# Kernel tuning notes

Hardware: AMD Instinct MI355X
Metric: run time of the kernel (lower is better)

## Reference

```python
import jax, jax.numpy as jnp
import numpy as np

D_MODEL = 1024
NUM_HEADS = 16
HEAD_DIM = D_MODEL // NUM_HEADS
SEQ_LEN = 2048
THETA = 10000.0


def setup_inputs() -> dict:
    key = jax.random.key(0)
    ks = jax.random.split(key, 9)
    s = 1.0 / np.sqrt(D_MODEL)
    inp = {
        "x": jax.random.normal(ks[0], (2, SEQ_LEN, D_MODEL), dtype=jnp.float32),
        "Wq": jax.random.uniform(ks[1], (D_MODEL, D_MODEL), jnp.float32, -s, s),
        "bq": jax.random.uniform(ks[2], (D_MODEL,), jnp.float32, -s, s),
        "Wk": jax.random.uniform(ks[3], (D_MODEL, D_MODEL), jnp.float32, -s, s),
        "bk": jax.random.uniform(ks[4], (D_MODEL,), jnp.float32, -s, s),
        "Wv": jax.random.uniform(ks[5], (D_MODEL, D_MODEL), jnp.float32, -s, s),
        "bv": jax.random.uniform(ks[6], (D_MODEL,), jnp.float32, -s, s),
        "Wo": jax.random.uniform(ks[7], (D_MODEL, D_MODEL), jnp.float32, -s, s),
        "bo": jax.random.uniform(ks[8], (D_MODEL,), jnp.float32, -s, s),
    }
    return inp


def _rope_cos_sin(seq_len, dim, theta):
    inv_freq = 1.0 / theta ** (jnp.arange(0, dim, 2, dtype=jnp.float32) / dim)  # [dim/2]
    t = jnp.arange(seq_len, dtype=jnp.float32)
    freqs = jnp.outer(t, inv_freq)  # [S, dim/2]
    return jnp.cos(freqs), jnp.sin(freqs)


def _apply_rope(x, cos, sin):
    # x: [B, H, S, head_dim]; interleaved complex pairs (even, odd)
    x2 = x.reshape(*x.shape[:-1], -1, 2)  # [B,H,S,hd/2,2]
    xe, xo = x2[..., 0], x2[..., 1]
    c = cos[None, None, :, :]
    s = sin[None, None, :, :]
    oe = xe * c - xo * s
    oo = xe * s + xo * c
    return jnp.stack([oe, oo], axis=-1).reshape(x.shape)


def reference(x, Wq, bq, Wk, bk, Wv, bv, Wo, bo):
    B, S, D = x.shape
    H, hd = NUM_HEADS, HEAD_DIM
    q = x @ Wq.T + bq
    k = x @ Wk.T + bk
    v = x @ Wv.T + bv
    # [B, H, S, hd]
    q = q.reshape(B, S, H, hd).transpose(0, 2, 1, 3)
    k = k.reshape(B, S, H, hd).transpose(0, 2, 1, 3)
    v = v.reshape(B, S, H, hd).transpose(0, 2, 1, 3)
    cos, sin = _rope_cos_sin(S, hd, THETA)
    q = _apply_rope(q, cos, sin)
    k = _apply_rope(k, cos, sin)
    scores = jnp.einsum("bhqd,bhkd->bhqk", q, k) / jnp.sqrt(jnp.float32(hd))
    causal = jnp.triu(jnp.ones((S, S), dtype=bool), k=1)
    scores = jnp.where(causal[None, None, :, :], -jnp.inf, scores)
    attn = jax.nn.softmax(scores, axis=-1)
    out = jnp.einsum("bhqk,bhkd->bhqd", attn, v)
    out = out.transpose(0, 2, 1, 3).reshape(B, S, D)
    return out @ Wo.T + bo
```

## Files before the change

### kernel.cpp

```cpp
#include <hip/hip_runtime.h>
#include <hip/hip_bf16.h>

#define S_LEN 2048
#define DM 1024
#define NH 16
#define HD 64
#define M_ROWS 4096
#define LOG2E 1.4426950408889634f
#define MASKVAL -1.0e4f
#define QSCALE 0.18033688011112042f

typedef __attribute__((ext_vector_type(8))) short short8;
typedef __attribute__((ext_vector_type(4))) float f32x4;
typedef __attribute__((ext_vector_type(16))) float f32x16;

__device__ inline ushort f2b(float f) {
  union { float f; unsigned u; } v; v.f = f;
  unsigned r = v.u + 0x7fffu + ((v.u >> 16) & 1u);
  return (ushort)(r >> 16);
}

__device__ inline float b2f(ushort u) {
  union { unsigned u; float f; } v; v.u = ((unsigned)u) << 16; return v.f;
}

__device__ inline unsigned pk_bf16(float a, float b) {
  __hip_bfloat162 h = __float22bfloat162_rn(make_float2(a, b));
  union { __hip_bfloat162 h; unsigned u; } v; v.h = h;
  return v.u;
}

__device__ inline float fexp2(float x) { return __builtin_amdgcn_exp2f(x); }

__device__ inline void gl_lds16(const void* g, void* l) {
  __builtin_amdgcn_global_load_lds(
      (const __attribute__((address_space(1))) void*)g,
      (__attribute__((address_space(3))) void*)l, 16, 0, 0);
}

__global__ __launch_bounds__(256) void cast_rope_kernel(
    const float* __restrict__ x, const float* __restrict__ Wq, const float* __restrict__ Wk,
    const float* __restrict__ Wv, const float* __restrict__ Wo,
    ushort* __restrict__ xb, ushort* __restrict__ Wqb, ushort* __restrict__ Wkb,
    ushort* __restrict__ Wvb, ushort* __restrict__ Wob,
    float* __restrict__ ropeC, float* __restrict__ ropeS) {
  const int bid = blockIdx.x;
  if (bid >= 8192) {
    int idx = (bid - 8192) * 256 + threadIdx.x;
    int s = idx >> 5, i = idx & 31;
    float inv = exp2f(-(float)i * (13.287712379549449f / 32.0f));
    float a = (float)s * inv;
    ropeC[idx] = cosf(a);
    ropeS[idx] = sinf(a);
    return;
  }
  int i = bid * 256 + threadIdx.x;
  int r = i >> 18, off = i & 0x3FFFF;
  const float4* s;
  uint2* d;
  switch (r) {
    case 0: case 1: case 2: case 3: s = (const float4*)x + i;  d = (uint2*)xb + i;  break;
    case 4: s = (const float4*)Wq + off; d = (uint2*)Wqb + off; break;
    case 5: s = (const float4*)Wk + off; d = (uint2*)Wkb + off; break;
    case 6: s = (const float4*)Wv + off; d = (uint2*)Wvb + off; break;
    default: s = (const float4*)Wo + off; d = (uint2*)Wob + off; break;
  }
  float4 v = *s;
  uint2 o;
  o.x = pk_bf16(v.x, v.y);
  o.y = pk_bf16(v.z, v.w);
  *d = o;
}

__global__ __launch_bounds__(256) void gemm_qkv_kernel(const ushort* __restrict__ xb,
    const ushort* __restrict__ Wqb, const ushort* __restrict__ Wkb, const ushort* __restrict__ Wvb,
    const float* __restrict__ bq, const float* __restrict__ bk, const float* __restrict__ bv,
    const float* __restrict__ ropeC, const float* __restrict__ ropeS,
    ushort* __restrict__ qb, ushort* __restrict__ kb, ushort* __restrict__ vT) {
  __shared__ ushort lds[17408];
  ushort* As = lds;
  ushort* Bs = lds + 8192;
  const int z = blockIdx.z;
  const ushort* W = (z == 0) ? Wqb : ((z == 1) ? Wkb : Wvb);
  const float* bias = (z == 0) ? bq : ((z == 1) ? bk : bv);
  const int m0 = blockIdx.x * 128, n0 = blockIdx.y * 128;
  const int t = threadIdx.x, lane = t & 63, wave = t >> 6;
  const int wr = (wave >> 1) * 64, wc = (wave & 1) * 64;
  const int lr = lane & 15, lg = lane >> 4;

  const int slot0 = wave * 128 + lane, slot1 = slot0 + 64;
  const int row0 = slot0 >> 2, g0 = (slot0 & 3) ^ (row0 & 3);
  const int row1 = slot1 >> 2, g1 = (slot1 & 3) ^ (row1 & 3);
  const ushort* Ap0 = &xb[(size_t)(m0 + row0) * DM + g0 * 8];
  const ushort* Ap1 = &xb[(size_t)(m0 + row1) * DM + g1 * 8];
  const ushort* Wp0 = &W[(size_t)(n0 + row0) * DM + g0 * 8];
  const ushort* Wp1 = &W[(size_t)(n0 + row1) * DM + g1 * 8];

  f32x4 acc[4][4];
#pragma unroll
  for (int a = 0; a < 4; a++)
#pragma unroll
    for (int b = 0; b < 4; b++) acc[a][b] = (f32x4){0.f, 0.f, 0.f, 0.f};

  gl_lds16(Ap0, &As[slot0 * 8]);
  gl_lds16(Ap1, &As[slot1 * 8]);
  gl_lds16(Wp0, &Bs[slot0 * 8]);
  gl_lds16(Wp1, &Bs[slot1 * 8]);
  __syncthreads();

  int buf = 0;
  for (int i = 0; i < 32; i++) {
    if (i + 1 < 32) {
      const int k0 = (i + 1) * 32;
      const int bo = (buf ^ 1) * 4096;
      gl_lds16(Ap0 + k0, &As[bo + slot0 * 8]);
      gl_lds16(Ap1 + k0, &As[bo + slot1 * 8]);
      gl_lds16(Wp0 + k0, &Bs[bo + slot0 * 8]);
      gl_lds16(Wp1 + k0, &Bs[bo + slot1 * 8]);
    }
    const int fb = buf * 4096;
    short8 af[4], bf[4];
#pragma unroll
    for (int mt = 0; mt < 4; mt++) {
      const int row = wr + mt * 16 + lr;
      af[mt] = *(const short8*)&As[fb + (row * 4 + (lg ^ (row & 3))) * 8];
    }
#pragma unroll
    for (int nt = 0; nt < 4; nt++) {
      const int row = wc + nt * 16 + lr;
      bf[nt] = *(const short8*)&Bs[fb + (row * 4 + (lg ^ (row & 3))) * 8];
    }
#pragma unroll
    for (int mt = 0; mt < 4; mt++)
#pragma unroll
      for (int nt = 0; nt < 4; nt++)
        acc[mt][nt] = __builtin_amdgcn_mfma_f32_16x16x32_bf16(af[mt], bf[nt], acc[mt][nt], 0, 0, 0);
    __syncthreads();
    buf ^= 1;
  }

#pragma unroll
  for (int mt = 0; mt < 4; mt++) {
#pragma unroll
    for (int nt = 0; nt < 4; nt++) {
      const int nloc = wc + nt * 16 + lr;
      const float bn = bias[n0 + nloc];
#pragma unroll
      for (int r = 0; r < 4; r++) {
        const int mloc = wr + mt * 16 + lg * 4 + r;
        const ushort v = f2b(acc[mt][nt][r] + bn);
        if (z < 2) lds[mloc * 136 + nloc] = v;
        else       lds[nloc * 136 + mloc] = v;
      }
    }
  }
  __syncthreads();

  const int b = m0 >> 11;
  if (z < 2) {
    ushort* dst = (z == 0) ? qb : kb;
    const float qscale = (z == 0) ? QSCALE : 1.0f;
#pragma unroll
    for (int c = 0; c < 8; c++) {
      const int sloc = c * 16 + (t >> 4);
      const int nloc = (t & 15) * 8;
      short8 val = *(const short8*)&lds[sloc * 136 + nloc];
      const int s = (m0 + sloc) & (S_LEN - 1);
      const int h = (n0 + nloc) >> 6;
      const int d0 = nloc & 63;
      const float4 cv = *(const float4*)&ropeC[s * 32 + d0 / 2];
      const float4 sv = *(const float4*)&ropeS[s * 32 + d0 / 2];
      uint4 o;
      {
        float e = b2f((ushort)val[0]), od = b2f((ushort)val[1]);
        o.x = pk_bf16((e * cv.x - od * sv.x) * qscale, (e * sv.x + od * cv.x) * qscale);
      }
      {
        float e = b2f((ushort)val[2]), od = b2f((ushort)val[3]);
        o.y = pk_bf16((e * cv.y - od * sv.y) * qscale, (e * sv.y + od * cv.y) * qscale);
      }
      {
        float e = b2f((ushort)val[4]), od = b2f((ushort)val[5]);
        o.z = pk_bf16((e * cv.z - od * sv.z) * qscale, (e * sv.z + od * cv.z) * qscale);
      }
      {
        float e = b2f((ushort)val[6]), od = b2f((ushort)val[7]);
        o.w = pk_bf16((e * cv.w - od * sv.w) * qscale, (e * sv.w + od * cv.w) * qscale);
      }
      *(uint4*)&dst[(((size_t)b * NH + h) * S_LEN + s) * HD + d0] = o;
    }
  } else {
    const int sbase = m0 & (S_LEN - 1);
#pragma unroll
    for (int c = 0; c < 8; c++) {
      const int nloc = c * 16 + (t >> 4);
      const int s0 = (t & 15) * 8;
      short8 val = *(const short8*)&lds[nloc * 136 + s0];
      const int h = (n0 + nloc) >> 6;
      const int d = nloc & 63;
      *(short8*)&vT[(((size_t)b * NH + h) * HD + d) * S_LEN + sbase + s0] = val;
    }
  }
}

__global__ __launch_bounds__(256) void flash_kernel(const ushort* __restrict__ qb,
                                                    const ushort* __restrict__ kb,
                                                    const ushort* __restrict__ vT,
                                                    ushort* __restrict__ Oh,
                                                    float* __restrict__ lsum) {
  __shared__ ushort Ks[2][4096];
  __shared__ ushort VTs[2][4096];
  const int t = threadIdx.x, lane = t & 63, wave = t >> 6;
  const int q31 = lane & 31, h = lane >> 5;
  const int bh = blockIdx.y;
  const int cid = blockIdx.x;
  const int g = (cid >= 24) ? 3 : (cid >= 12) ? 2 : (cid >= 4) ? 1 : 0;
  const int nc = g + 1;
  const int o = cid - 4 * ((g * (g + 1)) >> 1);
  const int qi = o / nc;
  const int c = o - qi * nc;
  const int qt = g * 4 + qi;
  const int q0 = qt * 128;
  const int ntiles = 2 * qt + 2;
  const int kstart = c * 8;
  const int kend = min(kstart + 8, ntiles);
  const int pidx = bh * 40 + cid;

  const ushort* kbh = kb + (size_t)bh * S_LEN * HD;
  const ushort* vbh = vT + (size_t)bh * HD * S_LEN;

  const int qrow = q0 + wave * 32 + q31;
  const ushort* qptr = qb + ((size_t)bh * S_LEN + qrow) * HD + h * 8;
  short8 qf[4];
#pragma unroll
  for (int s = 0; s < 4; s++) qf[s] = *(const short8*)(qptr + s * 16);

  const int slot0 = wave * 128 + lane, slot1 = slot0 + 64;
  const int row0 = slot0 >> 3, g0 = (slot0 & 7) ^ (row0 & 7);
  const int row1 = slot1 >> 3, g1 = (slot1 & 7) ^ (row1 & 7);
  const int lo0 = wave * 128 * 8, lo1 = lo0 + 64 * 8;

  int foff[4][2];
#pragma unroll
  for (int s = 0; s < 4; s++)
#pragma unroll
    for (int st = 0; st < 2; st++) {
      const int row = st * 32 + q31;
      foff[s][st] = (row * 8 + ((2 * s + h) ^ (row & 7))) * 8;
    }

  {
    const int k00 = kstart * 64;
    gl_lds16(kbh + (size_t)(k00 + row0) * HD + g0 * 8, &Ks[0][lo0]);
    gl_lds16(kbh + (size_t)(k00 + row1) * HD + g1 * 8, &Ks[0][lo1]);
    gl_lds16(vbh + (size_t)row0 * S_LEN + k00 + g0 * 8, &VTs[0][lo0]);
    gl_lds16(vbh + (size_t)row1 * S_LEN + k00 + g1 * 8, &VTs[0][lo1]);
  }
  __syncthreads();

  f32x16 O[2];
#pragma unroll
  for (int st = 0; st < 2; st++)
#pragma unroll
    for (int r = 0; r < 16; r++) O[st][r] = 0.f;
  float lacc = 0.f;
  int cur = 0;

  for (int kt = kstart; kt < kend; kt++) {
    if (kt + 1 < kend) {
      const int k0n = (kt + 1) * 64;
      gl_lds16(kbh + (size_t)(k0n + row0) * HD + g0 * 8, &Ks[cur ^ 1][lo0]);
      gl_lds16(kbh + (size_t)(k0n + row1) * HD + g1 * 8, &Ks[cur ^ 1][lo1]);
      gl_lds16(vbh + (size_t)row0 * S_LEN + k0n + g0 * 8, &VTs[cur ^ 1][lo0]);
      gl_lds16(vbh + (size_t)row1 * S_LEN + k0n + g1 * 8, &VTs[cur ^ 1][lo1]);
    }
    const ushort* Kb = Ks[cur];
    const ushort* Vb = VTs[cur];

    f32x16 sc[2];
#pragma unroll
    for (int st = 0; st < 2; st++)
#pragma unroll
      for (int r = 0; r < 16; r++) sc[st][r] = 0.f;
#pragma unroll
    for (int s = 0; s < 4; s++) {
#pragma unroll
      for (int st = 0; st < 2; st++) {
        const short8 kf = *(const short8*)&Kb[foff[s][st]];
        sc[st] = __builtin_amdgcn_mfma_f32_32x32x16_bf16(kf, qf[s], sc[st], 0, 0, 0);
      }
    }
    if (kt * 64 + 63 > q0 + wave * 32) {
#pragma unroll
      for (int st = 0; st < 2; st++)
#pragma unroll
        for (int r = 0; r < 16; r++) {
          const int kcol = kt * 64 + st * 32 + (r & 3) + 8 * (r >> 2) + 4 * h;
          if (kcol > qrow) sc[st][r] = MASKVAL;
        }
    }
#pragma unroll
    for (int st = 0; st < 2; st++)
#pragma unroll
      for (int r = 0; r < 16; r++) {
        const float p = fexp2(sc[st][r]);
        sc[st][r] = p;
        lacc += p;
      }

    unsigned pp[8][2];
#pragma unroll
    for (int st = 0; st < 2; st++)
#pragma unroll
      for (int rg = 0; rg < 4; rg++) {
        pp[st * 4 + rg][0] = pk_bf16(sc[st][4 * rg + 0], sc[st][4 * rg + 1]);
        pp[st * 4 + rg][1] = pk_bf16(sc[st][4 * rg + 2], sc[st][4 * rg + 3]);
      }
#pragma unroll
    for (int s = 0; s < 4; s++) {
      const unsigned sA0 = pp[2 * s][0], sA1 = pp[2 * s][1];
      const unsigned sB0 = pp[2 * s + 1][0], sB1 = pp[2 * s + 1][1];
      const unsigned send0 = h ? sA0 : sB0;
      const unsigned send1 = h ? sA1 : sB1;
      const unsigned recv0 = (unsigned)__shfl_xor((int)send0, 32);
      const unsigned recv1 = (unsigned)__shfl_xor((int)send1, 32);
      union { unsigned u[4]; short8 v; } pf;
      pf.u[0] = h ? recv0 : sA0;
      pf.u[1] = h ? recv1 : sA1;
      pf.u[2] = h ? sB0 : recv0;
      pf.u[3] = h ? sB1 : recv1;
#pragma unroll
      for (int st = 0; st < 2; st++) {
        const short8 vf = *(const short8*)&Vb[foff[s][st]];
        O[st] = __builtin_amdgcn_mfma_f32_32x32x16_bf16(vf, pf.v, O[st], 0, 0, 0);
      }
    }
    __syncthreads();
    cur ^= 1;
  }

  lacc += __shfl_xor(lacc, 32);

  ushort* obase = Oh + ((size_t)pidx * 128 + wave * 32 + q31) * HD;
#pragma unroll
  for (int st = 0; st < 2; st++)
#pragma unroll
    for (int rg = 0; rg < 4; rg++) {
      const int d0 = st * 32 + 8 * rg + 4 * h;
      uint2 w;
      w.x = pk_bf16(O[st][4 * rg + 0], O[st][4 * rg + 1]);
      w.y = pk_bf16(O[st][4 * rg + 2], O[st][4 * rg + 3]);
      *(uint2*)&obase[d0] = w;
    }
  if (h == 0) lsum[(size_t)pidx * 128 + wave * 32 + q31] = lacc;
}

__global__ __launch_bounds__(256) void combine_kernel(const ushort* __restrict__ Oh,
                                                      const float* __restrict__ lsum,
                                                      ushort* __restrict__ attn) {
  const int tid = blockIdx.x * 256 + threadIdx.x;
  const int d8 = tid & 7;
  const int q = (tid >> 3) & (S_LEN - 1);
  const int bh = tid >> 14;
  const int qt = q >> 7, row = q & 127;
  const int g = qt >> 2, nc = g + 1;
  const int base = 4 * ((g * (g + 1)) >> 1) + (qt & 3) * nc;
  const int p0 = bh * 40 + base;

  float l = 0.f;
  float acc[8];
#pragma unroll
  for (int j = 0; j < 8; j++) acc[j] = 0.f;
  for (int c = 0; c < nc; c++) {
    const size_t rowidx = (size_t)(p0 + c) * 128 + row;
    l += lsum[rowidx];
    const uint4 a = *(const uint4*)&Oh[rowidx * HD + d8 * 8];
    const unsigned au[4] = {a.x, a.y, a.z, a.w};
#pragma unroll
    for (int j = 0; j < 4; j++) {
      acc[2 * j] += b2f((ushort)(au[j] & 0xffff));
      acc[2 * j + 1] += b2f((ushort)(au[j] >> 16));
    }
  }
  const float inv = 1.f / l;
  uint4 o;
  unsigned* op = (unsigned*)&o;
#pragma unroll
  for (int j = 0; j < 4; j++) op[j] = pk_bf16(acc[2 * j] * inv, acc[2 * j + 1] * inv);
  const int b = bh >> 4, hh = bh & 15;
  *(uint4*)&attn[((size_t)b * S_LEN + q) * DM + hh * HD + d8 * 8] = o;
}

__global__ __launch_bounds__(256) void gemm_out_kernel(const ushort* __restrict__ attn,
                                                       const ushort* __restrict__ Wob,
                                                       const float* __restrict__ bo,
                                                       float* __restrict__ out) {
  __shared__ ushort As[2][4096];
  __shared__ ushort Bs[2][2048];
  const int m0 = blockIdx.x * 128, n0 = blockIdx.y * 64;
  const int t = threadIdx.x, lane = t & 63, wave = t >> 6;
  const int wm = (wave >> 1) * 64, wn = (wave & 1) * 32;
  const int lr = lane & 15, lg = lane >> 4;
  const int slotA0 = wave * 128 + lane, slotA1 = slotA0 + 64;
  const int rowA0 = slotA0 >> 2, gA0 = (slotA0 & 3) ^ (rowA0 & 3);
  const int rowA1 = slotA1 >> 2, gA1 = (slotA1 & 3) ^ (rowA1 & 3);
  const int slotB = wave * 64 + lane;
  const int rowB = slotB >> 2, gB = (slotB & 3) ^ (rowB & 3);
  const ushort* Ap0 = &attn[(size_t)(m0 + rowA0) * DM + gA0 * 8];
  const ushort* Ap1 = &attn[(size_t)(m0 + rowA1) * DM + gA1 * 8];
  const ushort* Wp  = &Wob[(size_t)(n0 + rowB) * DM + gB * 8];

  f32x4 acc[4][2];
#pragma unroll
  for (int a = 0; a < 4; a++)
#pragma unroll
    for (int b = 0; b < 2; b++) acc[a][b] = (f32x4){0.f, 0.f, 0.f, 0.f};

  gl_lds16(Ap0, &As[0][slotA0 * 8]);
  gl_lds16(Ap1, &As[0][slotA1 * 8]);
  gl_lds16(Wp, &Bs[0][slotB * 8]);
  __syncthreads();

  int buf = 0;
  for (int i = 0; i < 32; i++) {
    if (i + 1 < 32) {
      const int k0 = (i + 1) * 32;
      gl_lds16(Ap0 + k0, &As[buf ^ 1][slotA0 * 8]);
      gl_lds16(Ap1 + k0, &As[buf ^ 1][slotA1 * 8]);
      gl_lds16(Wp + k0, &Bs[buf ^ 1][slotB * 8]);
    }
    short8 af[4], bf[2];
#pragma unroll
    for (int mt = 0; mt < 4; mt++) {
      const int row = wm + mt * 16 + lr;
      af[mt] = *(const short8*)&As[buf][(row * 4 + (lg ^ (row & 3))) * 8];
    }
#pragma unroll
    for (int nt = 0; nt < 2; nt++) {
      const int row = wn + nt * 16 + lr;
      bf[nt] = *(const short8*)&Bs[buf][(row * 4 + (lg ^ (row & 3))) * 8];
    }
#pragma unroll
    for (int mt = 0; mt < 4; mt++)
#pragma unroll
      for (int nt = 0; nt < 2; nt++)
        acc[mt][nt] = __builtin_amdgcn_mfma_f32_16x16x32_bf16(af[mt], bf[nt], acc[mt][nt], 0, 0, 0);
    __syncthreads();
    buf ^= 1;
  }

#pragma unroll
  for (int mt = 0; mt < 4; mt++) {
#pragma unroll
    for (int nt = 0; nt < 2; nt++) {
      const int n = n0 + wn + nt * 16 + lr;
      const float bn = bo[n];
#pragma unroll
      for (int r = 0; r < 4; r++) {
        const int m = m0 + wm + mt * 16 + lg * 4 + r;
        out[(size_t)m * DM + n] = acc[mt][nt][r] + bn;
      }
    }
  }
}

extern "C" void kernel_launch(void* const* d_in, const int* in_sizes, int n_in,
                              void* d_out, int out_size, void* d_ws, size_t ws_size,
                              hipStream_t stream) {
  const float* x  = (const float*)d_in[0];
  const float* Wq = (const float*)d_in[1];
  const float* bq = (const float*)d_in[2];
  const float* Wk = (const float*)d_in[3];
  const float* bk = (const float*)d_in[4];
  const float* Wv = (const float*)d_in[5];
  const float* bv = (const float*)d_in[6];
  const float* Wo = (const float*)d_in[7];
  const float* bo = (const float*)d_in[8];
  float* out = (float*)d_out;

  char* ws = (char*)d_ws;
  size_t off = 0;
  auto alloc = [&](size_t bytes) { char* p = ws + off; off += (bytes + 255) & ~255ull; return p; };
  ushort* xb   = (ushort*)alloc((size_t)M_ROWS * DM * 2);
  ushort* Wqb  = (ushort*)alloc((size_t)DM * DM * 2);
  ushort* Wkb  = (ushort*)alloc((size_t)DM * DM * 2);
  ushort* Wvb  = (ushort*)alloc((size_t)DM * DM * 2);
  ushort* Wob  = (ushort*)alloc((size_t)DM * DM * 2);
  ushort* qb   = (ushort*)alloc((size_t)M_ROWS * DM * 2);
  ushort* kb   = (ushort*)alloc((size_t)M_ROWS * DM * 2);
  ushort* vTb  = (ushort*)alloc((size_t)M_ROWS * DM * 2);
  ushort* attn = (ushort*)alloc((size_t)M_ROWS * DM * 2);
  ushort* Ohb  = (ushort*)alloc((size_t)1280 * 128 * HD * 2);
  float* lsb   = (float*)alloc((size_t)1280 * 128 * 4);
  float* ropeC = (float*)alloc((size_t)S_LEN * 32 * 4);
  float* ropeS = (float*)alloc((size_t)S_LEN * 32 * 4);
  (void)ws_size; (void)in_sizes; (void)n_in; (void)out_size;

  cast_rope_kernel<<<8448, 256, 0, stream>>>(x, Wq, Wk, Wv, Wo, xb, Wqb, Wkb, Wvb, Wob,
                                             ropeC, ropeS);
  gemm_qkv_kernel<<<dim3(M_ROWS / 128, DM / 128, 3), 256, 0, stream>>>(
      xb, Wqb, Wkb, Wvb, bq, bk, bv, ropeC, ropeS, qb, kb, vTb);
  flash_kernel<<<dim3(40, 32), 256, 0, stream>>>(qb, kb, vTb, Ohb, lsb);
  combine_kernel<<<2048, 256, 0, stream>>>(Ohb, lsb, attn);
  gemm_out_kernel<<<dim3(M_ROWS / 128, DM / 64), 256, 0, stream>>>(attn, Wob, bo, out);
}
```

Before: 192.4 us.

## Unroll flash loop by two with static LDS offsets, permlane swap, and setprio

Rewrites the flash attention inner loop as a macro unrolled twice, so the double-buffer offsets into one flat LDS array become compile-time constants. Global pointers now advance by increment instead of being recomputed each tile. The cross-half exchange of P values uses v_permlane32_swap instead of two shuffles plus selects. s_setprio is raised around the MFMA blocks and the row sums are accumulated in packed two-wide vectors. The aim is lower address and exchange overhead and better MFMA issue. The risks are higher register pressure, and the tile count per block must be even because the second body in each pair runs without a bounds check.

Result: no change. 190.7 us (-0.9%).

```diff
diff --git a/kernel.cpp b/kernel.cpp
--- a/kernel.cpp
+++ b/kernel.cpp
@@ -11,6 +11,7 @@
 #define QSCALE 0.18033688011112042f
 
 typedef __attribute__((ext_vector_type(8))) short short8;
+typedef __attribute__((ext_vector_type(2))) float f32x2;
 typedef __attribute__((ext_vector_type(4))) float f32x4;
 typedef __attribute__((ext_vector_type(16))) float f32x16;
 
@@ -208,8 +209,7 @@
                                                     const ushort* __restrict__ vT,
                                                     ushort* __restrict__ Oh,
                                                     float* __restrict__ lsum) {
-  __shared__ ushort Ks[2][4096];
-  __shared__ ushort VTs[2][4096];
+  __shared__ ushort lds[16384];
   const int t = threadIdx.x, lane = t & 63, wave = t >> 6;
   const int q31 = lane & 31, h = lane >> 5;
   const int bh = blockIdx.y;
@@ -251,11 +251,15 @@
 
   {
     const int k00 = kstart * 64;
-    gl_lds16(kbh + (size_t)(k00 + row0) * HD + g0 * 8, &Ks[0][lo0]);
-    gl_lds16(kbh + (size_t)(k00 + row1) * HD + g1 * 8, &Ks[0][lo1]);
-    gl_lds16(vbh + (size_t)row0 * S_LEN + k00 + g0 * 8, &VTs[0][lo0]);
-    gl_lds16(vbh + (size_t)row1 * S_LEN + k00 + g1 * 8, &VTs[0][lo1]);
-  }
+    gl_lds16(kbh + (size_t)(k00 + row0) * HD + g0 * 8, &lds[0 + lo0]);
+    gl_lds16(kbh + (size_t)(k00 + row1) * HD + g1 * 8, &lds[0 + lo1]);
+    gl_lds16(vbh + (size_t)row0 * S_LEN + k00 + g0 * 8, &lds[8192 + lo0]);
+    gl_lds16(vbh + (size_t)row1 * S_LEN + k00 + g1 * 8, &lds[8192 + lo1]);
+  }
+  const ushort* kp0 = kbh + (size_t)(kstart * 64 + 64 + row0) * HD + g0 * 8;
+  const ushort* kp1 = kbh + (size_t)(kstart * 64 + 64 + row1) * HD + g1 * 8;
+  const ushort* vp0 = vbh + (size_t)row0 * S_LEN + kstart * 64 + 64 + g0 * 8;
+  const ushort* vp1 = vbh + (size_t)row1 * S_LEN + kstart * 64 + 64 + g1 * 8;
   __syncthreads();
 
   f32x16 O[2];
@@ -263,82 +267,89 @@
   for (int st = 0; st < 2; st++)
 #pragma unroll
     for (int r = 0; r < 16; r++) O[st][r] = 0.f;
-  float lacc = 0.f;
-  int cur = 0;
-
-  for (int kt = kstart; kt < kend; kt++) {
-    if (kt + 1 < kend) {
-      const int k0n = (kt + 1) * 64;
-      gl_lds16(kbh + (size_t)(k0n + row0) * HD + g0 * 8, &Ks[cur ^ 1][lo0]);
-      gl_lds16(kbh + (size_t)(k0n + row1) * HD + g1 * 8, &Ks[cur ^ 1][lo1]);
-      gl_lds16(vbh + (size_t)row0 * S_LEN + k0n + g0 * 8, &VTs[cur ^ 1][lo0]);
-      gl_lds16(vbh + (size_t)row1 * S_LEN + k0n + g1 * 8, &VTs[cur ^ 1][lo1]);
-    }
-    const ushort* Kb = Ks[cur];
-    const ushort* Vb = VTs[cur];
-
-    f32x16 sc[2];
-#pragma unroll
-    for (int st = 0; st < 2; st++)
-#pragma unroll
-      for (int r = 0; r < 16; r++) sc[st][r] = 0.f;
-#pragma unroll
-    for (int s = 0; s < 4; s++) {
-#pragma unroll
-      for (int st = 0; st < 2; st++) {
-        const short8 kf = *(const short8*)&Kb[foff[s][st]];
-        sc[st] = __builtin_amdgcn_mfma_f32_32x32x16_bf16(kf, qf[s], sc[st], 0, 0, 0);
-      }
-    }
-    if (kt * 64 + 63 > q0 + wave * 32) {
-#pragma unroll
-      for (int st = 0; st < 2; st++)
-#pragma unroll
-        for (int r = 0; r < 16; r++) {
-          const int kcol = kt * 64 + st * 32 + (r & 3) + 8 * (r >> 2) + 4 * h;
-          if (kcol > qrow) sc[st][r] = MASKVAL;
-        }
-    }
-#pragma unroll
-    for (int st = 0; st < 2; st++)
-#pragma unroll
-      for (int r = 0; r < 16; r++) {
-        const float p = fexp2(sc[st][r]);
-        sc[st][r] = p;
-        lacc += p;
-      }
-
-    unsigned pp[8][2];
-#pragma unroll
-    for (int st = 0; st < 2; st++)
-#pragma unroll
-      for (int rg = 0; rg < 4; rg++) {
-        pp[st * 4 + rg][0] = pk_bf16(sc[st][4 * rg + 0], sc[st][4 * rg + 1]);
-        pp[st * 4 + rg][1] = pk_bf16(sc[st][4 * rg + 2], sc[st][4 * rg + 3]);
-      }
-#pragma unroll
-    for (int s = 0; s < 4; s++) {
-      const unsigned sA0 = pp[2 * s][0], sA1 = pp[2 * s][1];
-      const unsigned sB0 = pp[2 * s + 1][0], sB1 = pp[2 * s + 1][1];
-      const unsigned send0 = h ? sA0 : sB0;
-      const unsigned send1 = h ? sA1 : sB1;
-      const unsigned recv0 = (unsigned)__shfl_xor((int)send0, 32);
-      const unsigned recv1 = (unsigned)__shfl_xor((int)send1, 32);
-      union { unsigned u[4]; short8 v; } pf;
-      pf.u[0] = h ? recv0 : sA0;
-      pf.u[1] = h ? recv1 : sA1;
-      pf.u[2] = h ? sB0 : recv0;
-      pf.u[3] = h ? sB1 : recv1;
-#pragma unroll
-      for (int st = 0; st < 2; st++) {
-        const short8 vf = *(const short8*)&Vb[foff[s][st]];
-        O[st] = __builtin_amdgcn_mfma_f32_32x32x16_bf16(vf, pf.v, O[st], 0, 0, 0);
-      }
-    }
-    __syncthreads();
-    cur ^= 1;
-  }
-
+
+  f32x16 zc;
+#pragma unroll
+  for (int r = 0; r < 16; r++) zc[r] = 0.f;
+
+  f32x2 lpA = (f32x2){0.f, 0.f}, lpB = (f32x2){0.f, 0.f};
+
+#define FLASH_BODY(KO, VO, PKO, PVO, KT, PREF)                                      \
+  {                                                                                 \
+    if (PREF) {                                                                     \
+      gl_lds16(kp0, &lds[(PKO) + lo0]);                                             \
+      gl_lds16(kp1, &lds[(PKO) + lo1]);                                             \
+      gl_lds16(vp0, &lds[(PVO) + lo0]);                                             \
+      gl_lds16(vp1, &lds[(PVO) + lo1]);                                             \
+      kp0 += 64 * HD; kp1 += 64 * HD; vp0 += 64; vp1 += 64;                         \
+    }                                                                               \
+    f32x16 sc0, sc1;                                                                \
+    __builtin_amdgcn_s_setprio(1);                                                  \
+    sc0 = __builtin_amdgcn_mfma_f32_32x32x16_bf16(                                  \
+        *(const short8*)&lds[(KO) + foff[0][0]], qf[0], zc, 0, 0, 0);               \
+    sc1 = __builtin_amdgcn_mfma_f32_32x32x16_bf16(                                  \
+        *(const short8*)&lds[(KO) + foff[0][1]], qf[0], zc, 0, 0, 0);               \
+    _Pragma("unroll")                                                               \
+    for (int s = 1; s < 4; s++) {                                                   \
+      sc0 = __builtin_amdgcn_mfma_f32_32x32x16_bf16(                                \
+          *(const short8*)&lds[(KO) + foff[s][0]], qf[s], sc0, 0, 0, 0);            \
+      sc1 = __builtin_amdgcn_mfma_f32_32x32x16_bf16(                                \
+          *(const short8*)&lds[(KO) + foff[s][1]], qf[s], sc1, 0, 0, 0);            \
+    }                                                                               \
+    __builtin_amdgcn_s_setprio(0);                                                  \
+    if ((KT) * 64 + 63 > q0 + wave * 32) {                                          \
+      _Pragma("unroll")                                                             \
+      for (int r = 0; r < 16; r++) {                                                \
+        const int kc0 = (KT) * 64 + (r & 3) + 8 * (r >> 2) + 4 * h;                 \
+        if (kc0 > qrow) sc0[r] = MASKVAL;                                           \
+        if (kc0 + 32 > qrow) sc1[r] = MASKVAL;                                      \
+      }                                                                             \
+    }                                                                               \
+    _Pragma("unroll")                                                               \
+    for (int r = 0; r < 16; r += 2) {                                               \
+      const float a0 = fexp2(sc0[r]), a1 = fexp2(sc0[r + 1]);                       \
+      const float b0 = fexp2(sc1[r]), b1 = fexp2(sc1[r + 1]);                       \
+      sc0[r] = a0; sc0[r + 1] = a1;                                                 \
+      sc1[r] = b0; sc1[r + 1] = b1;                                                 \
+      lpA += (f32x2){a0, a1};                                                       \
+      lpB += (f32x2){b0, b1};                                                       \
+    }                                                                               \
+    unsigned pp[8][2];                                                              \
+    _Pragma("unroll")                                                               \
+    for (int rg = 0; rg < 4; rg++) {                                                \
+      pp[rg][0] = pk_bf16(sc0[4 * rg + 0], sc0[4 * rg + 1]);                        \
+      pp[rg][1] = pk_bf16(sc0[4 * rg + 2], sc0[4 * rg + 3]);                        \
+      pp[4 + rg][0] = pk_bf16(sc1[4 * rg + 0], sc1[4 * rg + 1]);                    \
+      pp[4 + rg][1] = pk_bf16(sc1[4 * rg + 2], sc1[4 * rg + 3]);                    \
+    }                                                                               \
+    __builtin_amdgcn_s_setprio(1);                                                  \
+    _Pragma("unroll")                                                               \
+    for (int s = 0; s < 4; s++) {                                                   \
+      unsigned d0 = pp[2 * s][0], e0 = pp[2 * s + 1][0];                            \
+      unsigned d1 = pp[2 * s][1], e1 = pp[2 * s + 1][1];                            \
+      asm("v_permlane32_swap_b32 %0, %1" : "+v"(d0), "+v"(e0));                     \
+      asm("v_permlane32_swap_b32 %0, %1" : "+v"(d1), "+v"(e1));                     \
+      union { unsigned u[4]; short8 v; } pf;                                        \
+      pf.u[0] = d0;                                                                 \
+      pf.u[1] = d1;                                                                 \
+      pf.u[2] = e0;                                                                 \
+      pf.u[3] = e1;                                                                 \
+      O[0] = __builtin_amdgcn_mfma_f32_32x32x16_bf16(                               \
+          *(const short8*)&lds[(VO) + foff[s][0]], pf.v, O[0], 0, 0, 0);            \
+      O[1] = __builtin_amdgcn_mfma_f32_32x32x16_bf16(                               \
+          *(const short8*)&lds[(VO) + foff[s][1]], pf.v, O[1], 0, 0, 0);            \
+    }                                                                               \
+    __builtin_amdgcn_s_setprio(0);                                                  \
+    __syncthreads();                                                                \
+  }
+
+  for (int kt = kstart; kt < kend; kt += 2) {
+    FLASH_BODY(0, 8192, 4096, 12288, kt, true);
+    FLASH_BODY(4096, 12288, 0, 8192, kt + 1, (kt + 2 < kend));
+  }
+#undef FLASH_BODY
+
+  float lacc = (lpA[0] + lpA[1]) + (lpB[0] + lpB[1]);
   lacc += __shfl_xor(lacc, 32);
 
   ushort* obase = Oh + ((size_t)pidx * 128 + wave * 32 + q31) * HD;
```
